# Kernel optimization log

Hardware: AMD Instinct MI355X
Metric: run time of the kernel (lower is better)

## Reference

```python
import jax, jax.numpy as jnp
import numpy as np

BLOCK = 256
EPS = 1e-6

def _silu(x):
    return x * jax.nn.sigmoid(x)

def setup_inputs() -> dict:
    key = jax.random.key(0)
    k1, k2, k3, k4 = jax.random.split(key, 4)
    embed_dim, hidden_dim = 2048, 2048
    b, n, h = 2, 4096, 16
    x = jax.random.normal(k1, (b, n, embed_dim), dtype=jnp.float32)
    slope_rate = jax.random.uniform(k2, (h, 1, 1), dtype=jnp.float32, minval=0.01, maxval=1.0)
    W_qkvu = jax.random.normal(k3, (4 * hidden_dim, embed_dim), dtype=jnp.float32) / np.sqrt(embed_dim)
    W_out = jax.random.normal(k4, (embed_dim, hidden_dim), dtype=jnp.float32) / np.sqrt(hidden_dim)
    return {"x": x, "slope_rate": slope_rate, "W_qkvu": W_qkvu, "W_out": W_out}

def reference(x, slope_rate, W_qkvu, W_out):
    b, n, embed_dim = x.shape
    h = slope_rate.shape[0]
    hidden_dim = W_qkvu.shape[0] // 4
    d = hidden_dim // h  # head dim
    NB = n // BLOCK

    qkvu = x @ W_qkvu.T  # [b, n, 4*hidden]
    q, k, v, u = jnp.split(qkvu, 4, axis=-1)

    def to_heads(t):
        return t.reshape(b, n, h, d).transpose(0, 2, 1, 3)  # b h n d

    q = _silu(to_heads(q))
    k = _silu(to_heads(k))
    v = to_heads(v)

    s = slope_rate  # (h,1,1)
    arr = jnp.arange(1, BLOCK + 1, dtype=x.dtype)  # 1..BLOCK
    q_decay = jnp.exp(-s * arr[:, None])                 # (h, B, 1)
    k_decay = jnp.exp(-s * (BLOCK - arr[:, None]))       # (h, B, 1)
    idx = arr[:, None] - arr[None, :]                    # (B, B)
    diag_decay = jnp.exp(jnp.where(idx >= 0, -s * idx, -jnp.inf))  # (h, B, B)
    block_decay = jnp.exp(-s * BLOCK)                    # (h,1,1)

    # reshape into blocks, scan-major axis first
    def blk(t):
        return t.reshape(b, h, NB, BLOCK, d).transpose(2, 0, 1, 3, 4)

    qb, kb, vb = blk(q), blk(k), blk(v)

    def step(kv, inp):
        qi, ki, vi = inp  # (b,h,B,d)
        qkv_none_diag = jnp.einsum('bhmd,bhde->bhme', qi * q_decay, kv)
        qk = jnp.einsum('bhmd,bhsd->bhms', qi, ki) * diag_decay
        qkv_diag = jnp.einsum('bhms,bhse->bhme', qk, vi)
        kv_new = block_decay * kv + jnp.einsum('bhsd,bhse->bhde', ki * k_decay, vi)
        return kv_new, qkv_none_diag + qkv_diag

    kv0 = jnp.zeros((b, h, d, d), dtype=jnp.float32)
    _, outs = jax.lax.scan(step, kv0, (qb, kb, vb))  # (NB,b,h,B,d)

    o = outs.transpose(1, 2, 0, 3, 4).reshape(b, h, n, d)
    o = o.transpose(0, 2, 1, 3).reshape(b, n, hidden_dim)  # b n (h d)

    # simple RMSNorm (no learned scale)
    o = o * jax.lax.rsqrt(jnp.mean(o * o, axis=-1, keepdims=True) + EPS)
    o = u * o
    return o @ W_out.T
```

## Files before the change

### kernel.cpp

```cpp
#include <hip/hip_runtime.h>
#include <stdint.h>

#define GK 2048

typedef short s16x8 __attribute__((ext_vector_type(8)));
typedef short s16x4 __attribute__((ext_vector_type(4)));
typedef float fx4   __attribute__((ext_vector_type(4)));
typedef unsigned int ux2 __attribute__((ext_vector_type(2)));

#define SB0 __builtin_amdgcn_sched_barrier(0)

__device__ __forceinline__ float b2f(unsigned short s) {
  union { unsigned int u; float f; } x; x.u = ((unsigned int)s) << 16; return x.f;
}
__device__ __forceinline__ unsigned short f2b(float f) {
  union { float f; unsigned int u; } x; x.f = f;
  return (unsigned short)((x.u + 0x7fffu + ((x.u >> 16) & 1u)) >> 16);
}
__device__ __forceinline__ void gl_lds16(const void* g, void* l) {
  __builtin_amdgcn_global_load_lds(
      (const __attribute__((address_space(1))) void*)g,
      (__attribute__((address_space(3))) void*)l, 16, 0, 0);
}

__global__ __launch_bounds__(256, 4) void cvt_bf16(const float* __restrict__ in,
                                                   unsigned short* __restrict__ out) {
  int i = blockIdx.x * 256 + threadIdx.x;
  fx4 v = *(const fx4*)(in + (size_t)i * 4);
  ux2 p;
  p[0] = (unsigned int)f2b(v[0]) | ((unsigned int)f2b(v[1]) << 16);
  p[1] = (unsigned int)f2b(v[2]) | ((unsigned int)f2b(v[3]) << 16);
  *(ux2*)(out + (size_t)i * 4) = p;
}

__global__ __launch_bounds__(256, 4) void cvt2_bf16(
    const float* __restrict__ a, unsigned short* __restrict__ oa, int na4,
    const float* __restrict__ b, unsigned short* __restrict__ ob) {
  int i = blockIdx.x * 256 + threadIdx.x;
  const float* src; unsigned short* dst; int j;
  if (i < na4) { src = a; dst = oa; j = i; }
  else         { src = b; dst = ob; j = i - na4; }
  fx4 v = *(const fx4*)(src + (size_t)j * 4);
  ux2 p;
  p[0] = (unsigned int)f2b(v[0]) | ((unsigned int)f2b(v[1]) << 16);
  p[1] = (unsigned int)f2b(v[2]) | ((unsigned int)f2b(v[3]) << 16);
  *(ux2*)(dst + (size_t)j * 4) = p;
}

__global__ void sentinel_k(float* o, float val) { o[threadIdx.x] = val; }

template<int EPI>
__global__ __launch_bounds__(512, 2) void gemm8(
    const unsigned short* __restrict__ A, const unsigned short* __restrict__ B,
    int NT, int nBase,
    unsigned short* __restrict__ qp, unsigned short* __restrict__ kp,
    unsigned short* __restrict__ vp, unsigned short* __restrict__ up,
    float* __restrict__ Cf) {
  __shared__ __align__(16) unsigned short lds8[65536];
  const int nwg = gridDim.x;
  const int bid0 = blockIdx.x;
  const int cpx = nwg >> 3;
  const int bid = (bid0 & 7) * cpx + (bid0 >> 3);
  const int bm = bid / NT, bn = bid % NT;
  const int tid = threadIdx.x;
  const int w = tid >> 6, l = tid & 63;
  const int wr = w >> 2, wc = w & 3;
  const int g = l >> 4, li = l & 15;

  const int srow = l >> 3;
  const int scol = ((l & 7) ^ srow) << 3;
  const unsigned short* Asrc = A + (size_t)(bm * 256) * GK + scol;
  const unsigned short* Bsrc = B + (size_t)(bn * 256) * GK + scol;

  auto stA = [&](int bu, int h, int kt) {
    const unsigned short* s = Asrc + (size_t)(h * 128 + w * 8 + srow) * GK + kt;
    unsigned short* d = &lds8[(bu * 2 + h) * 8192 + w * 512];
    gl_lds16(s, d);
    gl_lds16(s + (size_t)64 * GK, d + 4096);
  };
  auto stB = [&](int bu, int h, int kt) {
    const unsigned short* s = Bsrc + (size_t)(h * 128 + w * 8 + srow) * GK + kt;
    unsigned short* d = &lds8[32768 + (bu * 2 + h) * 8192 + w * 512];
    gl_lds16(s, d);
    gl_lds16(s + (size_t)64 * GK, d + 4096);
  };

  const int s7 = li & 7;
  const int cb0 = ((0 + g) ^ s7) << 3;
  const int cb1 = ((4 + g) ^ s7) << 3;
  const int rbase = li * 64;
  const int Abase0 = wr * 8192;
  const int Bbase0 = 32768 + (wc >> 1) * 8192 + (wc & 1) * 4096;

  s16x8 aF[4][2], bL[2][2], bH[2][2];
  fx4 acc[8][4] = {};

  auto rdA = [&](int rb, int mh) {
    #pragma unroll
    for (int i = 0; i < 4; ++i) {
      int a0 = rb * 16384 + Abase0 + (mh * 4 + i) * 1024 + rbase;
      aF[i][0] = *(const s16x8*)&lds8[a0 + cb0];
      aF[i][1] = *(const s16x8*)&lds8[a0 + cb1];
    }
  };
  auto rdBL = [&](int rb) {
    #pragma unroll
    for (int i = 0; i < 2; ++i) {
      int a0 = rb * 16384 + Bbase0 + i * 1024 + rbase;
      bL[i][0] = *(const s16x8*)&lds8[a0 + cb0];
      bL[i][1] = *(const s16x8*)&lds8[a0 + cb1];
    }
  };
  auto rdBH = [&](int rb) {
    #pragma unroll
    for (int i = 0; i < 2; ++i) {
      int a0 = rb * 16384 + Bbase0 + (2 + i) * 1024 + rbase;
      bH[i][0] = *(const s16x8*)&lds8[a0 + cb0];
      bH[i][1] = *(const s16x8*)&lds8[a0 + cb1];
    }
  };
  auto mm = [&](int mh, int nh, s16x8 (&bF)[2][2]) {
    __builtin_amdgcn_s_setprio(1);
    #pragma unroll
    for (int i = 0; i < 4; ++i)
      #pragma unroll
      for (int j = 0; j < 2; ++j)
        #pragma unroll
        for (int kk = 0; kk < 2; ++kk)
          acc[mh * 4 + i][nh * 2 + j] =
              __builtin_amdgcn_mfma_f32_16x16x32_bf16(aF[i][kk], bF[j][kk],
                                                      acc[mh * 4 + i][nh * 2 + j], 0, 0, 0);
    __builtin_amdgcn_s_setprio(0);
  };

  const int KT = GK / 64;

  stA(0, 0, 0); stB(0, 0, 0); stA(0, 1, 0); stB(0, 1, 0);

  #pragma unroll 2
  for (int t = 0; t < KT - 1; ++t) {
    const int rb = t & 1, wb = rb ^ 1;
    const int ktn = (t + 1) * 64;
    stA(wb, 0, ktn);
    asm volatile("s_waitcnt vmcnt(2)" ::: "memory");
    SB0; __builtin_amdgcn_s_barrier(); SB0;
    rdA(rb, 0); rdBL(rb);
    mm(0, 0, bL);
    SB0; __builtin_amdgcn_s_barrier(); SB0;
    rdBH(rb);
    stB(wb, 0, ktn);
    SB0; __builtin_amdgcn_s_barrier(); SB0;
    mm(0, 1, bH);
    SB0; __builtin_amdgcn_s_barrier(); SB0;
    rdA(rb, 1);
    stA(wb, 1, ktn);
    SB0; __builtin_amdgcn_s_barrier(); SB0;
    mm(1, 1, bH);
    SB0; __builtin_amdgcn_s_barrier(); SB0;
    stB(wb, 1, ktn);
    SB0; __builtin_amdgcn_s_barrier(); SB0;
    mm(1, 0, bL);
    SB0; __builtin_amdgcn_s_barrier(); SB0;
  }
  {
    const int rb = (KT - 1) & 1;
    asm volatile("s_waitcnt vmcnt(0)" ::: "memory");
    SB0; __builtin_amdgcn_s_barrier(); SB0;
    rdA(rb, 0); rdBL(rb);
    mm(0, 0, bL);
    rdBH(rb);
    mm(0, 1, bH);
    rdA(rb, 1);
    mm(1, 1, bH);
    mm(1, 0, bL);
  }

  if (EPI == 0 || EPI == 2) {
    const int colbase = nBase + bn * 256 + wc * 64;
    #pragma unroll
    for (int mf = 0; mf < 8; ++mf)
      #pragma unroll
      for (int rr = 0; rr < 4; ++rr) {
        int row = bm * 256 + wr * 128 + mf * 16 + g * 4 + rr;
        int nn = row, bb = 0;
        if (EPI == 2) { bb = row >> 12; nn = row & 4095; }
        size_t boff = (size_t)bb * 8388608;
        #pragma unroll
        for (int nf = 0; nf < 4; ++nf) {
          int colglob = colbase + nf * 16 + li;
          int tq = colglob >> 11, hh = (colglob >> 7) & 15, cl = colglob & 127;
          float vv = acc[mf][nf][rr];
          if (tq < 2) vv = vv / (1.f + __expf(-vv));
          if (tq == 3) up[boff + (size_t)nn * 2048 + hh * 128 + cl] = f2b(vv);
          else ((tq == 0) ? qp : (tq == 1) ? kp : vp)[boff + ((size_t)hh * 4096 + nn) * 128 + cl] = f2b(vv);
        }
      }
  } else {
    #pragma unroll
    for (int mf = 0; mf < 8; ++mf)
      #pragma unroll
      for (int rr = 0; rr < 4; ++rr) {
        int row = bm * 256 + wr * 128 + mf * 16 + g * 4 + rr;
        #pragma unroll
        for (int nf = 0; nf < 4; ++nf) {
          int col = bn * 256 + wc * 64 + nf * 16 + li;
          Cf[(size_t)row * 2048 + col] = acc[mf][nf][rr];
        }
      }
  }
}

__global__ __launch_bounds__(256, 2) void gemm_out(
    const unsigned short* __restrict__ A, const unsigned short* __restrict__ B,
    float* __restrict__ Cf) {
  __shared__ __align__(16) short lA[128 * 64];
  __shared__ __align__(16) short lB[128 * 64];
  const int nwg = gridDim.x;
  const int bid0 = blockIdx.x;
  const int cpx = nwg >> 3;
  const int bid = (bid0 & 7) * cpx + (bid0 >> 3);
  const int bm = bid / 16, bn = bid % 16;
  const int tid = threadIdx.x;
  const int w = tid >> 6, l = tid & 63;
  const int wr = w >> 1, wc = w & 1;
  const int g = l >> 4, li = l & 15;

  fx4 acc[4][4] = {};
  const int aRow = l >> 3, aCol = (l & 7) * 8;
  const unsigned short* Abase = A + (size_t)(bm * 128) * GK + aCol;
  const unsigned short* Bbase = B + (size_t)(bn * 128) * GK + aCol;

  for (int kt = 0; kt < GK; kt += 64) {
    __syncthreads();
    #pragma unroll
    for (int j = 0; j < 4; ++j) {
      int c = w * 4 + j;
      gl_lds16(Abase + (size_t)(c * 8 + aRow) * GK + kt, &lA[c * 512]);
      gl_lds16(Bbase + (size_t)(c * 8 + aRow) * GK + kt, &lB[c * 512]);
    }
    __syncthreads();
    #pragma unroll
    for (int kk = 0; kk < 2; ++kk) {
      s16x8 af[4], bf[4];
      #pragma unroll
      for (int mf = 0; mf < 4; ++mf)
        af[mf] = *(const s16x8*)&lA[(wr * 64 + mf * 16 + li) * 64 + kk * 32 + g * 8];
      #pragma unroll
      for (int nf = 0; nf < 4; ++nf)
        bf[nf] = *(const s16x8*)&lB[(wc * 64 + nf * 16 + li) * 64 + kk * 32 + g * 8];
      #pragma unroll
      for (int mf = 0; mf < 4; ++mf)
        #pragma unroll
        for (int nf = 0; nf < 4; ++nf)
          acc[mf][nf] = __builtin_amdgcn_mfma_f32_16x16x32_bf16(af[mf], bf[nf], acc[mf][nf], 0, 0, 0);
    }
  }
  #pragma unroll
  for (int mf = 0; mf < 4; ++mf)
    #pragma unroll
    for (int rr = 0; rr < 4; ++rr) {
      int row = bm * 128 + wr * 64 + mf * 16 + g * 4 + rr;
      #pragma unroll
      for (int nf = 0; nf < 4; ++nf) {
        int col = bn * 128 + wc * 64 + nf * 16 + li;
        Cf[(size_t)row * 2048 + col] = acc[mf][nf][rr];
      }
    }
}

__global__ __launch_bounds__(256, 1) void pass1_C(
    const unsigned short* __restrict__ k, const unsigned short* __restrict__ v,
    const float* __restrict__ slope, float* __restrict__ C) {
  __shared__ __align__(16) unsigned short lK[256 * 128];
  __shared__ __align__(16) unsigned short lV[256 * 128];
  __shared__ float ldecay[256];
  const int bid = blockIdx.x;
  const int h_i = bid >> 4, ib = bid & 15;
  const int tid = threadIdx.x, w = tid >> 6, l = tid & 63;
  const int g = l >> 4, li = l & 15;
  const float r = slope[h_i];
  const size_t kvoff = ((size_t)h_i * 4096 + ib * 256) * 128;
  #pragma unroll
  for (int j = 0; j < 16; ++j) {
    int c = w * 16 + j;
    gl_lds16(k + kvoff + c * 512 + l * 8, &lK[c * 512]);
    gl_lds16(v + kvoff + c * 512 + l * 8, &lV[c * 512]);
  }
  ldecay[tid] = __expf(-r * (float)(255 - tid));
  __syncthreads();

  fx4 acc[2][8] = {};
  #pragma unroll 1
  for (int ks = 0; ks < 8; ++ks) {
    s16x8 a[2], b[8];
    #pragma unroll
    for (int mf = 0; mf < 2; ++mf) {
      int dr = w * 32 + mf * 16 + li;
      #pragma unroll
      for (int e = 0; e < 8; ++e) {
        int s = ks * 32 + g * 8 + e;
        a[mf][e] = (short)f2b(b2f(lK[s * 128 + dr]) * ldecay[s]);
      }
    }
    #pragma unroll
    for (int nf = 0; nf < 8; ++nf) {
      int er = nf * 16 + li;
      #pragma unroll
      for (int e = 0; e < 8; ++e) {
        int s = ks * 32 + g * 8 + e;
        b[nf][e] = (short)lV[s * 128 + er];
      }
    }
    #pragma unroll
    for (int mf = 0; mf < 2; ++mf)
      #pragma unroll
      for (int nf = 0; nf < 8; ++nf)
        acc[mf][nf] = __builtin_amdgcn_mfma_f32_16x16x32_bf16(a[mf], b[nf], acc[mf][nf], 0, 0, 0);
  }
  float* Cb = C + (size_t)bid * 16384;
  #pragma unroll
  for (int mf = 0; mf < 2; ++mf)
    #pragma unroll
    for (int rr = 0; rr < 4; ++rr)
      #pragma unroll
      for (int nf = 0; nf < 8; ++nf)
        Cb[(w * 32 + mf * 16 + g * 4 + rr) * 128 + nf * 16 + li] = acc[mf][nf][rr];
}

__global__ __launch_bounds__(256, 4) void scan_kv2(
    const float* __restrict__ C, const float* __restrict__ slope,
    unsigned short* __restrict__ KVb) {
  __shared__ unsigned short lds[8][128];
  const int h_i = blockIdx.x >> 4, c = blockIdx.x & 15;
  const float r = slope[h_i];
  const float bd = __expf(-256.f * r);
  const int t = threadIdx.x;
  float run[4] = {0.f, 0.f, 0.f, 0.f};
  const int e_out = t >> 1, dg = t & 1;
  for (int i = 0; i < 16; ++i) {
    size_t base = ((size_t)h_i * 16 + i) * 16384;
    fx4 cv = *(const fx4*)(C + base + c * 1024 + t * 4);
    #pragma unroll
    for (int j = 0; j < 4; ++j) lds[t >> 5][(t & 31) * 4 + j] = f2b(run[j]);
    __syncthreads();
    s16x4 ov;
    #pragma unroll
    for (int j = 0; j < 4; ++j) ov[j] = (short)lds[dg * 4 + j][e_out];
    *(s16x4*)&KVb[base + e_out * 128 + c * 8 + dg * 4] = ov;
    __syncthreads();
    #pragma unroll
    for (int j = 0; j < 4; ++j) run[j] = bd * run[j] + cv[j];
  }
}

__global__ __launch_bounds__(256, 1) void pass3_O(
    const unsigned short* __restrict__ q, const unsigned short* __restrict__ k,
    const unsigned short* __restrict__ v, const unsigned short* __restrict__ KVb,
    const float* __restrict__ slope, unsigned short* __restrict__ o) {
  __shared__ __align__(16) unsigned short lK[64 * 128];
  __shared__ __align__(16) unsigned short lV[64 * 128];
  __shared__ __align__(16) unsigned short lP[4 * 64 * 64];
  const int bid = blockIdx.x;
  const int h_i = bid >> 4, ib = bid & 15;
  const int n0 = ib * 256;
  const float r = slope[h_i];
  const int tid = threadIdx.x, w = tid >> 6, l = tid & 63;
  const int g = l >> 4, li = l & 15;
  const int mbase = w * 64;

  fx4 accO[4][8] = {};
  const unsigned short* Qb = q + ((size_t)h_i * 4096 + n0 + mbase) * 128;
  const unsigned short* KVbase = KVb + ((size_t)h_i * 16 + ib) * 16384;

  #pragma unroll
  for (int kd = 0; kd < 4; ++kd) {
    s16x8 aq[4], bkv[8];
    #pragma unroll
    for (int mf = 0; mf < 4; ++mf)
      aq[mf] = *(const s16x8*)(Qb + (size_t)(mf * 16 + li) * 128 + kd * 32 + g * 8);
    #pragma unroll
    for (int nf = 0; nf < 8; ++nf)
      bkv[nf] = *(const s16x8*)(KVbase + (size_t)(nf * 16 + li) * 128 + kd * 32 + g * 8);
    #pragma unroll
    for (int mf = 0; mf < 4; ++mf)
      #pragma unroll
      for (int nf = 0; nf < 8; ++nf)
        accO[mf][nf] = __builtin_amdgcn_mfma_f32_16x16x32_bf16(aq[mf], bkv[nf], accO[mf][nf], 0, 0, 0);
  }
  #pragma unroll
  for (int mf = 0; mf < 4; ++mf)
    #pragma unroll
    for (int rr = 0; rr < 4; ++rr) {
      float f = __expf(-r * (float)(mbase + mf * 16 + g * 4 + rr + 1));
      #pragma unroll
      for (int nf = 0; nf < 8; ++nf) accO[mf][nf][rr] *= f;
    }

  for (int st = 0; st < 4; ++st) {
    __syncthreads();
    #pragma unroll
    for (int j = 0; j < 4; ++j) {
      int c = w * 4 + j;
      size_t roff = ((size_t)h_i * 4096 + n0 + st * 64) * 128 + c * 512 + l * 8;
      gl_lds16(k + roff, &lK[c * 512]);
      gl_lds16(v + roff, &lV[c * 512]);
    }
    __syncthreads();
    if (st > w) continue;

    fx4 sacc[4][4] = {};
    #pragma unroll
    for (int kd = 0; kd < 4; ++kd) {
      s16x8 aq[4], bk[4];
      #pragma unroll
      for (int mf = 0; mf < 4; ++mf)
        aq[mf] = *(const s16x8*)(Qb + (size_t)(mf * 16 + li) * 128 + kd * 32 + g * 8);
      #pragma unroll
      for (int nf = 0; nf < 4; ++nf)
        bk[nf] = *(const s16x8*)&lK[(nf * 16 + li) * 128 + kd * 32 + g * 8];
      #pragma unroll
      for (int mf = 0; mf < 4; ++mf)
        #pragma unroll
        for (int nf = 0; nf < 4; ++nf)
          sacc[mf][nf] = __builtin_amdgcn_mfma_f32_16x16x32_bf16(aq[mf], bk[nf], sacc[mf][nf], 0, 0, 0);
    }

    float f2v[4];
    #pragma unroll
    for (int nf = 0; nf < 4; ++nf) f2v[nf] = __expf(r * (float)(nf * 16 + li));
    unsigned short* lPw = &lP[w * 4096];
    #pragma unroll
    for (int mf = 0; mf < 4; ++mf)
      #pragma unroll
      for (int rr = 0; rr < 4; ++rr) {
        int Aoff = mbase - st * 64 + mf * 16 + g * 4 + rr;
        float f1 = __expf(-r * (float)Aoff);
        #pragma unroll
        for (int nf = 0; nf < 4; ++nf) {
          int sc = nf * 16 + li;
          float val = (Aoff >= sc) ? sacc[mf][nf][rr] * f1 * f2v[nf] : 0.f;
          lPw[(mf * 16 + g * 4 + rr) * 64 + sc] = f2b(val);
        }
      }

    #pragma unroll
    for (int ks = 0; ks < 2; ++ks) {
      s16x8 pa[4], vb[8];
      #pragma unroll
      for (int mf = 0; mf < 4; ++mf)
        pa[mf] = *(const s16x8*)&lPw[(mf * 16 + li) * 64 + ks * 32 + g * 8];
      #pragma unroll
      for (int nf = 0; nf < 8; ++nf) {
        int er = nf * 16 + li;
        #pragma unroll
        for (int e = 0; e < 8; ++e) {
          int s = ks * 32 + g * 8 + e;
          vb[nf][e] = (short)lV[s * 128 + er];
        }
      }
      #pragma unroll
      for (int mf = 0; mf < 4; ++mf)
        #pragma unroll
        for (int nf = 0; nf < 8; ++nf)
          accO[mf][nf] = __builtin_amdgcn_mfma_f32_16x16x32_bf16(pa[mf], vb[nf], accO[mf][nf], 0, 0, 0);
    }
  }

  #pragma unroll
  for (int mf = 0; mf < 4; ++mf)
    #pragma unroll
    for (int rr = 0; rr < 4; ++rr) {
      int nn = n0 + mbase + mf * 16 + g * 4 + rr;
      unsigned short* ob = o + (size_t)nn * 2048 + h_i * 128;
      #pragma unroll
      for (int nf = 0; nf < 8; ++nf)
        ob[nf * 16 + li] = f2b(accO[mf][nf][rr]);
    }
}

__global__ __launch_bounds__(256, 4) void norm_mul(
    const unsigned short* __restrict__ o, const unsigned short* __restrict__ u,
    unsigned short* __restrict__ z) {
  __shared__ float red[4];
  const int row = blockIdx.x, t = threadIdx.x;
  const size_t base = (size_t)row * 2048 + t * 8;
  s16x8 ov = *(const s16x8*)(o + base);
  float vals[8]; float ss = 0.f;
  #pragma unroll
  for (int j = 0; j < 8; ++j) { vals[j] = b2f((unsigned short)ov[j]); ss += vals[j] * vals[j]; }
  #pragma unroll
  for (int dl = 1; dl < 64; dl <<= 1) ss += __shfl_xor(ss, dl);
  if ((t & 63) == 0) red[t >> 6] = ss;
  __syncthreads();
  float tot = red[0] + red[1] + red[2] + red[3];
  float rs = rsqrtf(tot * (1.f / 2048.f) + 1e-6f);
  s16x8 uv = *(const s16x8*)(u + base);
  s16x8 zv;
  #pragma unroll
  for (int j = 0; j < 8; ++j)
    zv[j] = (short)f2b(vals[j] * b2f((unsigned short)uv[j]) * rs);
  *(s16x8*)(z + base) = zv;
}

extern "C" void kernel_launch(void* const* d_in, const int* in_sizes, int n_in,
                              void* d_out, int out_size, void* d_ws, size_t ws_size,
                              hipStream_t stream) {
  (void)in_sizes; (void)n_in; (void)out_size;
  const float* x     = (const float*)d_in[0];
  const float* slope = (const float*)d_in[1];
  const float* Wqkvu = (const float*)d_in[2];
  const float* Wout  = (const float*)d_in[3];
  float* out = (float*)d_out;

  const size_t NEED_MED   = 92274688ull;
  const size_t NEED_BIG   = 125829120ull;
  const size_t NEED_HUGE  = 167772160ull;
  const size_t NEED_GIANT = 226492416ull;
  if (ws_size < NEED_MED) {
    sentinel_k<<<1, 256, 0, stream>>>(out, (float)((double)ws_size * 1e-6));
    return;
  }
  char* ws = (char*)d_ws;

  if (ws_size >= NEED_GIANT) {
    unsigned short* wq  = (unsigned short*)(ws + 0);
    unsigned short* xz  = (unsigned short*)(ws + 33554432);
    unsigned short* qb  = (unsigned short*)(ws + 67108864);
    unsigned short* kb  = (unsigned short*)(ws + 100663296);
    unsigned short* vb  = (unsigned short*)(ws + 134217728);
    unsigned short* ub  = (unsigned short*)(ws + 167772160);
    unsigned short* S0  = (unsigned short*)(ws + 201326592);
    unsigned short* KVr = (unsigned short*)(ws + 218103808);
    cvt2_bf16<<<32768, 256, 0, stream>>>(Wqkvu, wq, 4194304, x, xz);
    gemm8<2><<<1024, 512, 0, stream>>>(xz, wq, 32, 0, qb, kb, vb, ub, nullptr);
    for (int bb = 0; bb < 2; ++bb) {
      size_t boff = (size_t)bb * 8388608;
      pass1_C<<<256, 256, 0, stream>>>(kb + boff, vb + boff, slope, (float*)S0);
      scan_kv2<<<256, 256, 0, stream>>>((float*)S0, slope, KVr);
      pass3_O<<<256, 256, 0, stream>>>(qb + boff, kb + boff, vb + boff, KVr, slope, S0);
      norm_mul<<<4096, 256, 0, stream>>>(S0, ub + boff, xz + boff);
    }
    cvt_bf16<<<4096, 256, 0, stream>>>(Wout, KVr);
    gemm8<1><<<256, 512, 0, stream>>>(xz, KVr, 8, 0,
                                      nullptr, nullptr, nullptr, nullptr, out);
  } else if (ws_size >= NEED_HUGE) {
    unsigned short* wq  = (unsigned short*)(ws + 0);
    unsigned short* xz  = (unsigned short*)(ws + 33554432);
    unsigned short* qb  = (unsigned short*)(ws + 67108864);
    unsigned short* kb  = (unsigned short*)(ws + 83886080);
    unsigned short* vb  = (unsigned short*)(ws + 100663296);
    unsigned short* ub  = (unsigned short*)(ws + 117440512);
    unsigned short* S0  = (unsigned short*)(ws + 134217728);
    unsigned short* KVr = (unsigned short*)(ws + 150994944);
    cvt2_bf16<<<32768, 256, 0, stream>>>(Wqkvu, wq, 4194304, x, xz);
    for (int bb = 0; bb < 2; ++bb) {
      unsigned short* xzb = xz + (size_t)bb * 8388608;
      gemm8<0><<<512, 512, 0, stream>>>(xzb, wq, 32, 0, qb, kb, vb, ub, nullptr);
      pass1_C<<<256, 256, 0, stream>>>(kb, vb, slope, (float*)S0);
      scan_kv2<<<256, 256, 0, stream>>>((float*)S0, slope, KVr);
      pass3_O<<<256, 256, 0, stream>>>(qb, kb, vb, KVr, slope, S0);
      norm_mul<<<4096, 256, 0, stream>>>(S0, ub, xzb);
    }
    cvt_bf16<<<4096, 256, 0, stream>>>(Wout, KVr);
    gemm8<1><<<256, 512, 0, stream>>>(xz, KVr, 8, 0,
                                      nullptr, nullptr, nullptr, nullptr, out);
  } else if (ws_size >= NEED_BIG) {
    unsigned short* wq  = (unsigned short*)(ws + 0);
    unsigned short* S0  = (unsigned short*)(ws + 33554432);
    unsigned short* qb  = (unsigned short*)(ws + 50331648);
    unsigned short* kb  = (unsigned short*)(ws + 67108864);
    unsigned short* vb  = (unsigned short*)(ws + 83886080);
    unsigned short* ub  = (unsigned short*)(ws + 100663296);
    unsigned short* KVr = (unsigned short*)(ws + 117440512);
    cvt_bf16<<<16384, 256, 0, stream>>>(Wqkvu, wq);
    for (int bb = 0; bb < 2; ++bb) {
      const float* xB = x + (size_t)bb * 8388608;
      float* outB = out + (size_t)bb * 8388608;
      cvt_bf16<<<8192, 256, 0, stream>>>(xB, S0);
      gemm8<0><<<512, 512, 0, stream>>>(S0, wq, 32, 0, qb, kb, vb, ub, nullptr);
      pass1_C<<<256, 256, 0, stream>>>(kb, vb, slope, (float*)S0);
      scan_kv2<<<256, 256, 0, stream>>>((float*)S0, slope, KVr);
      pass3_O<<<256, 256, 0, stream>>>(qb, kb, vb, KVr, slope, S0);
      cvt_bf16<<<4096, 256, 0, stream>>>(Wout, KVr);
      norm_mul<<<4096, 256, 0, stream>>>(S0, ub, qb);
      gemm_out<<<512, 256, 0, stream>>>(qb, KVr, outB);
    }
  } else {
    unsigned short* reg0 = (unsigned short*)(ws + 0);
    unsigned short* qb   = (unsigned short*)(ws + 16777216);
    unsigned short* kb   = (unsigned short*)(ws + 33554432);
    unsigned short* vb   = (unsigned short*)(ws + 50331648);
    unsigned short* ub   = (unsigned short*)(ws + 67108864);
    unsigned short* KVr  = (unsigned short*)(ws + 83886080);
    for (int bb = 0; bb < 2; ++bb) {
      const float* xB = x + (size_t)bb * 8388608;
      float* outB = out + (size_t)bb * 8388608;
      cvt_bf16<<<8192, 256, 0, stream>>>(xB, reg0);
      cvt_bf16<<<8192, 256, 0, stream>>>(Wqkvu, vb);
      gemm8<0><<<256, 512, 0, stream>>>(reg0, vb, 16, 0, qb, kb, vb, ub, nullptr);
      cvt_bf16<<<4096, 256, 0, stream>>>(Wqkvu + 8388608, KVr);
      gemm8<0><<<128, 512, 0, stream>>>(reg0, KVr, 8, 4096, qb, kb, vb, ub, nullptr);
      cvt_bf16<<<4096, 256, 0, stream>>>(Wqkvu + 12582912, KVr);
      gemm8<0><<<128, 512, 0, stream>>>(reg0, KVr, 8, 6144, qb, kb, vb, ub, nullptr);
      pass1_C<<<256, 256, 0, stream>>>(kb, vb, slope, (float*)reg0);
      scan_kv2<<<256, 256, 0, stream>>>((float*)reg0, slope, KVr);
      pass3_O<<<256, 256, 0, stream>>>(qb, kb, vb, KVr, slope, reg0);
      norm_mul<<<4096, 256, 0, stream>>>(reg0, ub, qb);
      cvt_bf16<<<4096, 256, 0, stream>>>(Wout, reg0);
      gemm_out<<<512, 256, 0, stream>>>(qb, reg0, outB);
    }
  }
}
```

Baseline: 508.4 us.

## Batch both sequences per launch in linear-attention passes and fold Wout conversion into one cvt

The per-batch loop of pass1/scan/pass3/norm launches becomes single launches with twice the grid, where each block derives its batch from the high bits of blockIdx. The launches were 256 blocks with one block per CU, which underfills the GPU; doubling the grid aims to fill the CUs and halve the launch count. The Wout bf16 conversion is merged into a three-source conversion kernel, and the now-dead xz buffer is reused as scratch for C and the attention output, with norm_mul running in place. The risks are aliasing mistakes in the reused buffers and the in-place normalisation.

```diff
diff --git a/kernel.cpp b/kernel.cpp
--- a/kernel.cpp
+++ b/kernel.cpp
@@ -40,6 +40,22 @@
   const float* src; unsigned short* dst; int j;
   if (i < na4) { src = a; dst = oa; j = i; }
   else         { src = b; dst = ob; j = i - na4; }
+  fx4 v = *(const fx4*)(src + (size_t)j * 4);
+  ux2 p;
+  p[0] = (unsigned int)f2b(v[0]) | ((unsigned int)f2b(v[1]) << 16);
+  p[1] = (unsigned int)f2b(v[2]) | ((unsigned int)f2b(v[3]) << 16);
+  *(ux2*)(dst + (size_t)j * 4) = p;
+}
+
+__global__ __launch_bounds__(256, 4) void cvt3_bf16(
+    const float* __restrict__ a, unsigned short* __restrict__ oa, int na4,
+    const float* __restrict__ b, unsigned short* __restrict__ ob, int nb4,
+    const float* __restrict__ c, unsigned short* __restrict__ oc) {
+  int i = blockIdx.x * 256 + threadIdx.x;
+  const float* src; unsigned short* dst; int j;
+  if (i < na4)            { src = a; dst = oa; j = i; }
+  else if (i < na4 + nb4) { src = b; dst = ob; j = i - na4; }
+  else                    { src = c; dst = oc; j = i - na4 - nb4; }
   fx4 v = *(const fx4*)(src + (size_t)j * 4);
   ux2 p;
   p[0] = (unsigned int)f2b(v[0]) | ((unsigned int)f2b(v[1]) << 16);
@@ -274,7 +290,9 @@
   __shared__ __align__(16) unsigned short lK[256 * 128];
   __shared__ __align__(16) unsigned short lV[256 * 128];
   __shared__ float ldecay[256];
-  const int bid = blockIdx.x;
+  const int bb = blockIdx.x >> 8;
+  const int bid = blockIdx.x & 255;
+  k += (size_t)bb * 8388608; v += (size_t)bb * 8388608; C += (size_t)bb * 4194304;
   const int h_i = bid >> 4, ib = bid & 15;
   const int tid = threadIdx.x, w = tid >> 6, l = tid & 63;
   const int g = l >> 4, li = l & 15;
@@ -331,7 +349,10 @@
     const float* __restrict__ C, const float* __restrict__ slope,
     unsigned short* __restrict__ KVb) {
   __shared__ unsigned short lds[8][128];
-  const int h_i = blockIdx.x >> 4, c = blockIdx.x & 15;
+  const int bb = blockIdx.x >> 8;
+  const int bid = blockIdx.x & 255;
+  C += (size_t)bb * 4194304; KVb += (size_t)bb * 4194304;
+  const int h_i = bid >> 4, c = bid & 15;
   const float r = slope[h_i];
   const float bd = __expf(-256.f * r);
   const int t = threadIdx.x;
@@ -360,7 +381,10 @@
   __shared__ __align__(16) unsigned short lK[64 * 128];
   __shared__ __align__(16) unsigned short lV[64 * 128];
   __shared__ __align__(16) unsigned short lP[4 * 64 * 64];
-  const int bid = blockIdx.x;
+  const int bb = blockIdx.x >> 8;
+  const int bid = blockIdx.x & 255;
+  q += (size_t)bb * 8388608; k += (size_t)bb * 8388608; v += (size_t)bb * 8388608;
+  KVb += (size_t)bb * 4194304; o += (size_t)bb * 8388608;
   const int h_i = bid >> 4, ib = bid & 15;
   const int n0 = ib * 256;
   const float r = slope[h_i];
@@ -529,19 +553,17 @@
     unsigned short* kb  = (unsigned short*)(ws + 100663296);
     unsigned short* vb  = (unsigned short*)(ws + 134217728);
     unsigned short* ub  = (unsigned short*)(ws + 167772160);
-    unsigned short* S0  = (unsigned short*)(ws + 201326592);
-    unsigned short* KVr = (unsigned short*)(ws + 218103808);
-    cvt2_bf16<<<32768, 256, 0, stream>>>(Wqkvu, wq, 4194304, x, xz);
+    unsigned short* KV  = (unsigned short*)(ws + 201326592);
+    unsigned short* wo  = (unsigned short*)(ws + 218103808);
+    float*          Ca  = (float*)xz;
+    unsigned short* oa  = xz;
+    cvt3_bf16<<<36864, 256, 0, stream>>>(Wqkvu, wq, 4194304, x, xz, 4194304, Wout, wo);
     gemm8<2><<<1024, 512, 0, stream>>>(xz, wq, 32, 0, qb, kb, vb, ub, nullptr);
-    for (int bb = 0; bb < 2; ++bb) {
-      size_t boff = (size_t)bb * 8388608;
-      pass1_C<<<256, 256, 0, stream>>>(kb + boff, vb + boff, slope, (float*)S0);
-      scan_kv2<<<256, 256, 0, stream>>>((float*)S0, slope, KVr);
-      pass3_O<<<256, 256, 0, stream>>>(qb + boff, kb + boff, vb + boff, KVr, slope, S0);
-      norm_mul<<<4096, 256, 0, stream>>>(S0, ub + boff, xz + boff);
-    }
-    cvt_bf16<<<4096, 256, 0, stream>>>(Wout, KVr);
-    gemm8<1><<<256, 512, 0, stream>>>(xz, KVr, 8, 0,
+    pass1_C<<<512, 256, 0, stream>>>(kb, vb, slope, Ca);
+    scan_kv2<<<512, 256, 0, stream>>>(Ca, slope, KV);
+    pass3_O<<<512, 256, 0, stream>>>(qb, kb, vb, KV, slope, oa);
+    norm_mul<<<8192, 256, 0, stream>>>(oa, ub, oa);
+    gemm8<1><<<256, 512, 0, stream>>>(oa, wo, 8, 0,
                                       nullptr, nullptr, nullptr, nullptr, out);
   } else if (ws_size >= NEED_HUGE) {
     unsigned short* wq  = (unsigned short*)(ws + 0);
```

After: 502.0 us. About the same (-1.3%).
